# Optimization experiments

Hardware: AMD Instinct MI355X
Metric: run time of the kernel (lower is better)

The kernel has to match this reference:

```python
import jax, jax.numpy as jnp
import numpy as np

DEPTH = 10
B, F = 8192, 512
NUM_INTERNAL = 2 ** DEPTH - 1   # 1023
NUM_LEAVES = 2 ** DEPTH         # 1024
LEAF_DIMS = 64


def setup_inputs() -> dict:
    key = jax.random.key(0)
    k1, k2, k3 = jax.random.split(key, 3)
    x = jax.random.normal(k1, (B, F), dtype=jnp.float32)
    # All internal-node Dense(1) gates batched into one weight matrix [F, num_internal].
    W = jax.random.normal(k2, (F, NUM_INTERNAL), dtype=jnp.float32) * (1.0 / np.sqrt(F))
    b = jnp.zeros((NUM_INTERNAL,), dtype=jnp.float32)
    leaves_weights = jax.random.normal(k3, (NUM_LEAVES, LEAF_DIMS), dtype=jnp.float32)
    return {"x": x, "W": W, "b": b, "leaves_weights": leaves_weights}


def reference(x, W, b, leaves_weights):
    # All gate probabilities in one fused matmul + sigmoid: [B, num_internal].
    # Node i's gate is column i (BFS / level order, same as the original list of Dense layers).
    p = jax.nn.sigmoid(x @ W + b)
    batch = x.shape[0]
    # Level-by-level probability propagation. prob has shape [B, 2^lvl]:
    # the path probability of each node at the current level.
    prob = jnp.ones((batch, 1), dtype=x.dtype)
    for lvl in range(DEPTH):
        start = 2 ** lvl - 1                      # first node index at this level
        p_lvl = p[:, start:start + 2 ** lvl]      # [B, 2^lvl] gate probs at this level
        # left child gets p * prob, right child gets (1-p) * prob, interleaved in node order
        prob = jnp.stack([p_lvl * prob, (1.0 - p_lvl) * prob], axis=-1)
        prob = prob.reshape(batch, 2 ** (lvl + 1))
    # Leaf-weighted sum: sum_l prob[:, l] * leaves_weights[l, :] -> [B, leaf_dims]
    return prob @ leaves_weights
```

## Files before the change

### kernel.cpp

```cpp
#include <hip/hip_runtime.h>


typedef short bf16x8 __attribute__((ext_vector_type(8)));
typedef float f32x4 __attribute__((ext_vector_type(4)));

#define GLOAD16(g, l) __builtin_amdgcn_global_load_lds( \
    (const __attribute__((address_space(1))) void*)(g), \
    (__attribute__((address_space(3))) void*)(l), 16, 0, 0)

__device__ __forceinline__ unsigned short f2bf(float f) {
    unsigned u = __float_as_uint(f);
    return (unsigned short)((u + 0x7FFFu + ((u >> 16) & 1u)) >> 16);
}

__global__ __launch_bounds__(256) void convert_split(const float* __restrict__ x,
                                                     const float* __restrict__ W,
                                                     unsigned short* __restrict__ xh,
                                                     unsigned short* __restrict__ xl,
                                                     unsigned short* __restrict__ wh,
                                                     unsigned short* __restrict__ wl)
{
    __shared__ float tile[32][33];
    const int b = blockIdx.x;
    const int tid = threadIdx.x;
    if (b < 1024) {
        const float4* xs = reinterpret_cast<const float4*>(x);
        #pragma unroll
        for (int i = 0; i < 4; ++i) {
            const int idx = b * 1024 + i * 256 + tid;
            const float4 v = xs[idx];
            ushort4 h, l;
            h.x = f2bf(v.x); l.x = f2bf(v.x - __uint_as_float((unsigned)h.x << 16));
            h.y = f2bf(v.y); l.y = f2bf(v.y - __uint_as_float((unsigned)h.y << 16));
            h.z = f2bf(v.z); l.z = f2bf(v.z - __uint_as_float((unsigned)h.z << 16));
            h.w = f2bf(v.w); l.w = f2bf(v.w - __uint_as_float((unsigned)h.w << 16));
            reinterpret_cast<ushort4*>(xh)[idx] = h;
            reinterpret_cast<ushort4*>(xl)[idx] = l;
        }
    } else {
        const int tb = b - 1024;
        const int k0 = (tb >> 5) * 32;
        const int n0 = (tb & 31) * 32;
        const int tk = tid >> 5, tn = tid & 31;
        #pragma unroll
        for (int j = 0; j < 4; ++j) {
            const int k = k0 + tk + j * 8;
            const int n = n0 + tn;
            tile[tk + j * 8][tn] = (n < 1023) ? W[(size_t)k * 1023 + n] : 0.f;
        }
        __syncthreads();
        const int wn = tid >> 5, wk = tid & 31;
        #pragma unroll
        for (int j = 0; j < 4; ++j) {
            const int n = n0 + wn + j * 8;
            const float v = tile[wk][wn + j * 8];
            const unsigned short h = f2bf(v);
            const unsigned short lo = f2bf(v - __uint_as_float((unsigned)h << 16));
            wh[(size_t)n * 512 + k0 + wk] = h;
            wl[(size_t)n * 512 + k0 + wk] = lo;
        }
    }
}

__global__ __launch_bounds__(256, 2) void gemm_sig_mfma(
    const unsigned short* __restrict__ xh, const unsigned short* __restrict__ xl,
    const unsigned short* __restrict__ wh, const unsigned short* __restrict__ wl,
    const float* __restrict__ bias, float* __restrict__ p)
{
    __shared__ __align__(16) unsigned short Ah[128 * 32];
    __shared__ __align__(16) unsigned short Al[128 * 32];
    __shared__ __align__(16) unsigned short Bh[128 * 32];
    __shared__ __align__(16) unsigned short Bl[128 * 32];

    const int tid = threadIdx.x;
    const int lane = tid & 63;
    const int wv = tid >> 6;
    const int m_base = blockIdx.y * 128;
    const int n_base = blockIdx.x * 128;
    const int wr = wv >> 1, wc = wv & 1;

    f32x4 acc[4][4];
    #pragma unroll
    for (int i = 0; i < 4; ++i)
        #pragma unroll
        for (int j = 0; j < 4; ++j)
            acc[i][j] = (f32x4){0.f, 0.f, 0.f, 0.f};

    const int c0 = tid, c1 = tid + 256;
    const int lb0 = wv * 512;
    const int lb1 = 2048 + wv * 512;
    const int a0row = c0 >> 2, a0kc = (c0 & 3) * 8;
    const int a1row = c1 >> 2, a1kc = (c1 & 3) * 8;

    const int l15 = lane & 15, kg = lane >> 4;

    for (int k0 = 0; k0 < 512; k0 += 32) {
        GLOAD16(xh + (size_t)(m_base + a0row) * 512 + k0 + a0kc, Ah + lb0);
        GLOAD16(xh + (size_t)(m_base + a1row) * 512 + k0 + a1kc, Ah + lb1);
        GLOAD16(xl + (size_t)(m_base + a0row) * 512 + k0 + a0kc, Al + lb0);
        GLOAD16(xl + (size_t)(m_base + a1row) * 512 + k0 + a1kc, Al + lb1);
        GLOAD16(wh + (size_t)(n_base + a0row) * 512 + k0 + a0kc, Bh + lb0);
        GLOAD16(wh + (size_t)(n_base + a1row) * 512 + k0 + a1kc, Bh + lb1);
        GLOAD16(wl + (size_t)(n_base + a0row) * 512 + k0 + a0kc, Bl + lb0);
        GLOAD16(wl + (size_t)(n_base + a1row) * 512 + k0 + a1kc, Bl + lb1);
        __syncthreads();

        bf16x8 ah[4], al[4], bh[4], bl[4];
        #pragma unroll
        for (int mi = 0; mi < 4; ++mi) {
            const int off = (wr * 64 + mi * 16 + l15) * 32 + kg * 8;
            ah[mi] = *reinterpret_cast<const bf16x8*>(&Ah[off]);
            al[mi] = *reinterpret_cast<const bf16x8*>(&Al[off]);
        }
        #pragma unroll
        for (int ni = 0; ni < 4; ++ni) {
            const int off = (wc * 64 + ni * 16 + l15) * 32 + kg * 8;
            bh[ni] = *reinterpret_cast<const bf16x8*>(&Bh[off]);
            bl[ni] = *reinterpret_cast<const bf16x8*>(&Bl[off]);
        }
        #pragma unroll
        for (int mi = 0; mi < 4; ++mi)
            #pragma unroll
            for (int ni = 0; ni < 4; ++ni) {
                acc[mi][ni] = __builtin_amdgcn_mfma_f32_16x16x32_bf16(ah[mi], bh[ni], acc[mi][ni], 0, 0, 0);
                acc[mi][ni] = __builtin_amdgcn_mfma_f32_16x16x32_bf16(ah[mi], bl[ni], acc[mi][ni], 0, 0, 0);
                acc[mi][ni] = __builtin_amdgcn_mfma_f32_16x16x32_bf16(al[mi], bh[ni], acc[mi][ni], 0, 0, 0);
            }
        __syncthreads();
    }

    const int l4 = lane >> 4;
    #pragma unroll
    for (int ni = 0; ni < 4; ++ni) {
        const int n = n_base + wc * 64 + ni * 16 + l15;
        if (n < 1023) {
            const float bv = bias[n];
            #pragma unroll
            for (int mi = 0; mi < 4; ++mi) {
                #pragma unroll
                for (int r = 0; r < 4; ++r) {
                    const int m = m_base + wr * 64 + mi * 16 + l4 * 4 + r;
                    const float v = acc[mi][ni][r] + bv;
                    p[(size_t)m * 1024 + n] = 1.f / (1.f + __expf(-v));
                }
            }
        }
    }
}

__global__ __launch_bounds__(256, 4) void gemm_sig_f32(const float* __restrict__ x,
                                                       const float* __restrict__ W,
                                                       const float* __restrict__ bias,
                                                       float* __restrict__ p)
{
    __shared__ __align__(16) float As[16][128 + 4];
    __shared__ __align__(16) float Bs[16][64 + 4];
    const int tid = threadIdx.x;
    const int m_base = blockIdx.y * 128;
    const int n_base = blockIdx.x * 64;
    const int m0 = (tid >> 4) * 8, n0 = (tid & 15) * 4;
    float acc[8][4];
    #pragma unroll
    for (int i = 0; i < 8; ++i)
        #pragma unroll
        for (int j = 0; j < 4; ++j) acc[i][j] = 0.f;
    const int arow = tid >> 2, acol = (tid & 3) * 4;
    const int bk = tid >> 4, bn = (tid & 15) * 4;
    for (int k0 = 0; k0 < 512; k0 += 16) {
        #pragma unroll
        for (int i = 0; i < 2; ++i) {
            const int row = arow + i * 64;
            const float4 a = *reinterpret_cast<const float4*>(&x[(size_t)(m_base + row) * 512 + k0 + acol]);
            As[0][(acol + 0) * 132 + row] = a.x;
            As[0][(acol + 1) * 132 + row] = a.y;
            As[0][(acol + 2) * 132 + row] = a.z;
            As[0][(acol + 3) * 132 + row] = a.w;
        }
        {
            const int gk = k0 + bk;
            #pragma unroll
            for (int j = 0; j < 4; ++j) {
                const int gn = n_base + bn + j;
                Bs[bk][bn + j] = (gn < 1023) ? W[(size_t)gk * 1023 + gn] : 0.f;
            }
        }
        __syncthreads();
        #pragma unroll
        for (int kk = 0; kk < 16; ++kk) {
            const float4 b4 = *reinterpret_cast<const float4*>(&Bs[kk][n0]);
            const float4 a0 = *reinterpret_cast<const float4*>(&As[kk][m0]);
            const float4 a1 = *reinterpret_cast<const float4*>(&As[kk][m0 + 4]);
            const float a[8] = {a0.x, a0.y, a0.z, a0.w, a1.x, a1.y, a1.z, a1.w};
            const float b[4] = {b4.x, b4.y, b4.z, b4.w};
            #pragma unroll
            for (int i = 0; i < 8; ++i)
                #pragma unroll
                for (int j = 0; j < 4; ++j)
                    acc[i][j] = fmaf(a[i], b[j], acc[i][j]);
        }
        __syncthreads();
    }
    #pragma unroll
    for (int i = 0; i < 8; ++i) {
        const int gm = m_base + m0 + i;
        #pragma unroll
        for (int j = 0; j < 4; ++j) {
            const int gn = n_base + n0 + j;
            if (gn < 1023) {
                float v = acc[i][j] + bias[gn];
                p[(size_t)gm * 1024 + gn] = 1.0f / (1.0f + __expf(-v));
            }
        }
    }
}

__global__ __launch_bounds__(256, 4) void tree_leaves(const float* __restrict__ p,
                                                      const float* __restrict__ leaves,
                                                      float* __restrict__ out)
{
    __shared__ __align__(16) float prob[8][1024];

    const int tid = threadIdx.x;
    const int row_base = blockIdx.x * 8;
    const int r = tid >> 5, s = tid & 31;
    const float* pr = p + (size_t)(row_base + r) * 1024;

    float prefix = 1.f;
    #pragma unroll
    for (int lvl = 0; lvl < 5; ++lvl) {
        const int node = (1 << lvl) - 1 + (s >> (5 - lvl));
        const float v = pr[node];
        prefix *= ((s >> (4 - lvl)) & 1) ? (1.f - v) : v;
    }

    float q1[2], q2[4], q3[8], q4[16], q5[32];
    {
        const float v = pr[31 + s];
        q1[0] = prefix * v; q1[1] = prefix * (1.f - v);
    }
    {
        const float va = pr[63 + 2 * s], vb = pr[64 + 2 * s];
        q2[0] = q1[0] * va; q2[1] = q1[0] * (1.f - va);
        q2[2] = q1[1] * vb; q2[3] = q1[1] * (1.f - vb);
    }
    #pragma unroll
    for (int j = 0; j < 4; ++j) {
        const float v = pr[127 + 4 * s + j];
        q3[2 * j] = q2[j] * v; q3[2 * j + 1] = q2[j] * (1.f - v);
    }
    #pragma unroll
    for (int j = 0; j < 8; ++j) {
        const float v = pr[255 + 8 * s + j];
        q4[2 * j] = q3[j] * v; q4[2 * j + 1] = q3[j] * (1.f - v);
    }
    #pragma unroll
    for (int j = 0; j < 16; ++j) {
        const float v = pr[511 + 16 * s + j];
        q5[2 * j] = q4[j] * v; q5[2 * j + 1] = q4[j] * (1.f - v);
    }

    const int sw = (s & 7) << 2;
    #pragma unroll
    for (int u = 0; u < 32; u += 4) {
        float4 q; q.x = q5[u]; q.y = q5[u + 1]; q.z = q5[u + 2]; q.w = q5[u + 3];
        *reinterpret_cast<float4*>(&prob[r][s * 32 + (u ^ sw)]) = q;
    }
    __syncthreads();

    const int d = tid & 63, chunk = tid >> 6;
    float acc2[8];
    #pragma unroll
    for (int i = 0; i < 8; ++i) acc2[i] = 0.f;
    const float* lvp = leaves + (size_t)(chunk << 8) * 64 + d;
    for (int i = 0; i < 256; i += 4) {
        const float l0 = lvp[(i + 0) * 64];
        const float l1 = lvp[(i + 1) * 64];
        const float l2 = lvp[(i + 2) * 64];
        const float l3 = lvp[(i + 3) * 64];
        const int base = (chunk << 8) + i;
        const int sblk = base >> 5;
        const int addr = (sblk << 5) + ((base & 31) ^ ((sblk & 7) << 2));
        #pragma unroll
        for (int r2 = 0; r2 < 8; ++r2) {
            const float4 pv = *reinterpret_cast<const float4*>(&prob[r2][addr]);
            acc2[r2] = fmaf(pv.x, l0, acc2[r2]);
            acc2[r2] = fmaf(pv.y, l1, acc2[r2]);
            acc2[r2] = fmaf(pv.z, l2, acc2[r2]);
            acc2[r2] = fmaf(pv.w, l3, acc2[r2]);
        }
    }

    __syncthreads();
    float* red = &prob[0][0];
    #pragma unroll
    for (int r2 = 0; r2 < 8; ++r2)
        red[(chunk * 8 + r2) * 64 + d] = acc2[r2];
    __syncthreads();
    if (chunk == 0) {
        #pragma unroll
        for (int r2 = 0; r2 < 8; ++r2) {
            const float sum = red[r2 * 64 + d] + red[(8 + r2) * 64 + d]
                            + red[(16 + r2) * 64 + d] + red[(24 + r2) * 64 + d];
            out[(size_t)(row_base + r2) * 64 + d] = sum;
        }
    }
}

extern "C" void kernel_launch(void* const* d_in, const int* in_sizes, int n_in,
                              void* d_out, int out_size, void* d_ws, size_t ws_size,
                              hipStream_t stream) {
    const float* x      = (const float*)d_in[0];
    const float* W      = (const float*)d_in[1];
    const float* b      = (const float*)d_in[2];
    const float* leaves = (const float*)d_in[3];
    float* out = (float*)d_out;

    float* p = (float*)d_ws;
    const size_t NEED = 52428800;

    if (ws_size >= NEED) {
        unsigned short* xh = (unsigned short*)((char*)d_ws + 33554432);
        unsigned short* xl = (unsigned short*)((char*)d_ws + 41943040);
        unsigned short* wh = (unsigned short*)((char*)d_ws + 50331648);
        unsigned short* wl = (unsigned short*)((char*)d_ws + 51380224);
        convert_split<<<1536, 256, 0, stream>>>(x, W, xh, xl, wh, wl);
        gemm_sig_mfma<<<dim3(8, 64), 256, 0, stream>>>(xh, xl, wh, wl, b, p);
    } else {
        gemm_sig_f32<<<dim3(16, 64), 256, 0, stream>>>(x, W, b, p);
    }
    tree_leaves<<<1024, 256, 0, stream>>>(p, leaves, out);
}
```

Baseline: 135.2 us.

## Double-buffer GEMM LDS tiles, shift p layout for aligned loads, re-tile leaf sum

```diff
diff --git a/kernel.cpp b/kernel.cpp
--- a/kernel.cpp
+++ b/kernel.cpp
@@ -67,10 +67,10 @@
     const unsigned short* __restrict__ wh, const unsigned short* __restrict__ wl,
     const float* __restrict__ bias, float* __restrict__ p)
 {
-    __shared__ __align__(16) unsigned short Ah[128 * 32];
-    __shared__ __align__(16) unsigned short Al[128 * 32];
-    __shared__ __align__(16) unsigned short Bh[128 * 32];
-    __shared__ __align__(16) unsigned short Bl[128 * 32];
+    __shared__ __align__(16) unsigned short Ah[2][128 * 32];
+    __shared__ __align__(16) unsigned short Al[2][128 * 32];
+    __shared__ __align__(16) unsigned short Bh[2][128 * 32];
+    __shared__ __align__(16) unsigned short Bl[2][128 * 32];
 
     const int tid = threadIdx.x;
     const int lane = tid & 63;
@@ -91,32 +91,44 @@
     const int lb1 = 2048 + wv * 512;
     const int a0row = c0 >> 2, a0kc = (c0 & 3) * 8;
     const int a1row = c1 >> 2, a1kc = (c1 & 3) * 8;
-
     const int l15 = lane & 15, kg = lane >> 4;
 
-    for (int k0 = 0; k0 < 512; k0 += 32) {
-        GLOAD16(xh + (size_t)(m_base + a0row) * 512 + k0 + a0kc, Ah + lb0);
-        GLOAD16(xh + (size_t)(m_base + a1row) * 512 + k0 + a1kc, Ah + lb1);
-        GLOAD16(xl + (size_t)(m_base + a0row) * 512 + k0 + a0kc, Al + lb0);
-        GLOAD16(xl + (size_t)(m_base + a1row) * 512 + k0 + a1kc, Al + lb1);
-        GLOAD16(wh + (size_t)(n_base + a0row) * 512 + k0 + a0kc, Bh + lb0);
-        GLOAD16(wh + (size_t)(n_base + a1row) * 512 + k0 + a1kc, Bh + lb1);
-        GLOAD16(wl + (size_t)(n_base + a0row) * 512 + k0 + a0kc, Bl + lb0);
-        GLOAD16(wl + (size_t)(n_base + a1row) * 512 + k0 + a1kc, Bl + lb1);
-        __syncthreads();
+    const size_t ga0 = (size_t)(m_base + a0row) * 512 + a0kc;
+    const size_t ga1 = (size_t)(m_base + a1row) * 512 + a1kc;
+    const size_t gb0 = (size_t)(n_base + a0row) * 512 + a0kc;
+    const size_t gb1 = (size_t)(n_base + a1row) * 512 + a1kc;
+
+    #define STAGE(buf, k0) do { \
+        GLOAD16(xh + ga0 + (k0), &Ah[buf][lb0]); \
+        GLOAD16(xh + ga1 + (k0), &Ah[buf][lb1]); \
+        GLOAD16(xl + ga0 + (k0), &Al[buf][lb0]); \
+        GLOAD16(xl + ga1 + (k0), &Al[buf][lb1]); \
+        GLOAD16(wh + gb0 + (k0), &Bh[buf][lb0]); \
+        GLOAD16(wh + gb1 + (k0), &Bh[buf][lb1]); \
+        GLOAD16(wl + gb0 + (k0), &Bl[buf][lb0]); \
+        GLOAD16(wl + gb1 + (k0), &Bl[buf][lb1]); \
+    } while (0)
+
+    STAGE(0, 0);
+    __syncthreads();
+
+    #pragma unroll
+    for (int t = 0; t < 16; ++t) {
+        const int cur = t & 1;
+        if (t < 15) STAGE(cur ^ 1, (t + 1) * 32);
 
         bf16x8 ah[4], al[4], bh[4], bl[4];
         #pragma unroll
         for (int mi = 0; mi < 4; ++mi) {
             const int off = (wr * 64 + mi * 16 + l15) * 32 + kg * 8;
-            ah[mi] = *reinterpret_cast<const bf16x8*>(&Ah[off]);
-            al[mi] = *reinterpret_cast<const bf16x8*>(&Al[off]);
+            ah[mi] = *reinterpret_cast<const bf16x8*>(&Ah[cur][off]);
+            al[mi] = *reinterpret_cast<const bf16x8*>(&Al[cur][off]);
         }
         #pragma unroll
         for (int ni = 0; ni < 4; ++ni) {
             const int off = (wc * 64 + ni * 16 + l15) * 32 + kg * 8;
-            bh[ni] = *reinterpret_cast<const bf16x8*>(&Bh[off]);
-            bl[ni] = *reinterpret_cast<const bf16x8*>(&Bl[off]);
+            bh[ni] = *reinterpret_cast<const bf16x8*>(&Bh[cur][off]);
+            bl[ni] = *reinterpret_cast<const bf16x8*>(&Bl[cur][off]);
         }
         #pragma unroll
         for (int mi = 0; mi < 4; ++mi)
@@ -128,6 +140,7 @@
             }
         __syncthreads();
     }
+    #undef STAGE
 
     const int l4 = lane >> 4;
     #pragma unroll
@@ -141,7 +154,7 @@
                 for (int r = 0; r < 4; ++r) {
                     const int m = m_base + wr * 64 + mi * 16 + l4 * 4 + r;
                     const float v = acc[mi][ni][r] + bv;
-                    p[(size_t)m * 1024 + n] = 1.f / (1.f + __expf(-v));
+                    p[(size_t)m * 1024 + 1 + n] = 1.f / (1.f + __expf(-v));
                 }
             }
         }
@@ -208,7 +221,7 @@
             const int gn = n_base + n0 + j;
             if (gn < 1023) {
                 float v = acc[i][j] + bias[gn];
-                p[(size_t)gm * 1024 + gn] = 1.0f / (1.0f + __expf(-v));
+                p[(size_t)gm * 1024 + 1 + gn] = 1.0f / (1.0f + __expf(-v));
             }
         }
     }
@@ -228,35 +241,48 @@
     float prefix = 1.f;
     #pragma unroll
     for (int lvl = 0; lvl < 5; ++lvl) {
-        const int node = (1 << lvl) - 1 + (s >> (5 - lvl));
-        const float v = pr[node];
+        const float v = pr[(1 << lvl) + (s >> (5 - lvl))];
         prefix *= ((s >> (4 - lvl)) & 1) ? (1.f - v) : v;
     }
 
     float q1[2], q2[4], q3[8], q4[16], q5[32];
     {
-        const float v = pr[31 + s];
+        const float v = pr[32 + s];
         q1[0] = prefix * v; q1[1] = prefix * (1.f - v);
     }
     {
-        const float va = pr[63 + 2 * s], vb = pr[64 + 2 * s];
-        q2[0] = q1[0] * va; q2[1] = q1[0] * (1.f - va);
-        q2[2] = q1[1] * vb; q2[3] = q1[1] * (1.f - vb);
-    }
-    #pragma unroll
-    for (int j = 0; j < 4; ++j) {
-        const float v = pr[127 + 4 * s + j];
-        q3[2 * j] = q2[j] * v; q3[2 * j + 1] = q2[j] * (1.f - v);
-    }
-    #pragma unroll
-    for (int j = 0; j < 8; ++j) {
-        const float v = pr[255 + 8 * s + j];
-        q4[2 * j] = q3[j] * v; q4[2 * j + 1] = q3[j] * (1.f - v);
-    }
-    #pragma unroll
-    for (int j = 0; j < 16; ++j) {
-        const float v = pr[511 + 16 * s + j];
-        q5[2 * j] = q4[j] * v; q5[2 * j + 1] = q4[j] * (1.f - v);
+        const float2 v2 = *reinterpret_cast<const float2*>(&pr[64 + 2 * s]);
+        q2[0] = q1[0] * v2.x; q2[1] = q1[0] * (1.f - v2.x);
+        q2[2] = q1[1] * v2.y; q2[3] = q1[1] * (1.f - v2.y);
+    }
+    {
+        const float4 v4 = *reinterpret_cast<const float4*>(&pr[128 + 4 * s]);
+        const float v[4] = {v4.x, v4.y, v4.z, v4.w};
+        #pragma unroll
+        for (int j = 0; j < 4; ++j) {
+            q3[2 * j] = q2[j] * v[j]; q3[2 * j + 1] = q2[j] * (1.f - v[j]);
+        }
+    }
+    {
+        const float4 va = *reinterpret_cast<const float4*>(&pr[256 + 8 * s]);
+        const float4 vb = *reinterpret_cast<const float4*>(&pr[260 + 8 * s]);
+        const float v[8] = {va.x, va.y, va.z, va.w, vb.x, vb.y, vb.z, vb.w};
+        #pragma unroll
+        for (int j = 0; j < 8; ++j) {
+            q4[2 * j] = q3[j] * v[j]; q4[2 * j + 1] = q3[j] * (1.f - v[j]);
+        }
+    }
+    {
+        float v[16];
+        #pragma unroll
+        for (int u = 0; u < 4; ++u) {
+            const float4 vv = *reinterpret_cast<const float4*>(&pr[512 + 16 * s + 4 * u]);
+            v[4 * u] = vv.x; v[4 * u + 1] = vv.y; v[4 * u + 2] = vv.z; v[4 * u + 3] = vv.w;
+        }
+        #pragma unroll
+        for (int j = 0; j < 16; ++j) {
+            q5[2 * j] = q4[j] * v[j]; q5[2 * j + 1] = q4[j] * (1.f - v[j]);
+        }
     }
 
     const int sw = (s & 7) << 2;
@@ -267,42 +293,54 @@
     }
     __syncthreads();
 
-    const int d = tid & 63, chunk = tid >> 6;
-    float acc2[8];
-    #pragma unroll
-    for (int i = 0; i < 8; ++i) acc2[i] = 0.f;
-    const float* lvp = leaves + (size_t)(chunk << 8) * 64 + d;
-    for (int i = 0; i < 256; i += 4) {
-        const float l0 = lvp[(i + 0) * 64];
-        const float l1 = lvp[(i + 1) * 64];
-        const float l2 = lvp[(i + 2) * 64];
-        const float l3 = lvp[(i + 3) * 64];
-        const int base = (chunk << 8) + i;
-        const int sblk = base >> 5;
-        const int addr = (sblk << 5) + ((base & 31) ^ ((sblk & 7) << 2));
-        #pragma unroll
-        for (int r2 = 0; r2 < 8; ++r2) {
-            const float4 pv = *reinterpret_cast<const float4*>(&prob[r2][addr]);
-            acc2[r2] = fmaf(pv.x, l0, acc2[r2]);
-            acc2[r2] = fmaf(pv.y, l1, acc2[r2]);
-            acc2[r2] = fmaf(pv.z, l2, acc2[r2]);
-            acc2[r2] = fmaf(pv.w, l3, acc2[r2]);
-        }
-    }
+    const int cg = tid >> 4, dg = tid & 15;
+    float acc[8][4];
+    #pragma unroll
+    for (int i = 0; i < 8; ++i)
+        #pragma unroll
+        for (int j = 0; j < 4; ++j) acc[i][j] = 0.f;
+
+    const float* lv_base = leaves + (size_t)(cg * 64) * 64 + dg * 4;
+    #pragma unroll 4
+    for (int i4 = 0; i4 < 16; ++i4) {
+        const int l0 = cg * 64 + i4 * 4;
+        const int m_ = (cg * 2 + (i4 >> 3)) & 7;
+        const int col = (cg * 64 + ((i4 * 4) ^ (m_ << 2)));
+        float4 lv[4];
+        #pragma unroll
+        for (int j = 0; j < 4; ++j)
+            lv[j] = *reinterpret_cast<const float4*>(&leaves[(size_t)(l0 + j) * 64 + dg * 4]);
+        #pragma unroll
+        for (int rr = 0; rr < 8; ++rr) {
+            const float4 pv = *reinterpret_cast<const float4*>(&prob[rr][col]);
+            const float pvv[4] = {pv.x, pv.y, pv.z, pv.w};
+            #pragma unroll
+            for (int j = 0; j < 4; ++j) {
+                acc[rr][0] = fmaf(pvv[j], lv[j].x, acc[rr][0]);
+                acc[rr][1] = fmaf(pvv[j], lv[j].y, acc[rr][1]);
+                acc[rr][2] = fmaf(pvv[j], lv[j].z, acc[rr][2]);
+                acc[rr][3] = fmaf(pvv[j], lv[j].w, acc[rr][3]);
+            }
+        }
+    }
+    (void)lv_base;
 
     __syncthreads();
     float* red = &prob[0][0];
     #pragma unroll
-    for (int r2 = 0; r2 < 8; ++r2)
-        red[(chunk * 8 + r2) * 64 + d] = acc2[r2];
+    for (int rr = 0; rr < 8; ++rr) {
+        float4 q; q.x = acc[rr][0]; q.y = acc[rr][1]; q.z = acc[rr][2]; q.w = acc[rr][3];
+        *reinterpret_cast<float4*>(&red[(size_t)(cg * 8 + rr) * 64 + dg * 4]) = q;
+    }
     __syncthreads();
-    if (chunk == 0) {
-        #pragma unroll
-        for (int r2 = 0; r2 < 8; ++r2) {
-            const float sum = red[r2 * 64 + d] + red[(8 + r2) * 64 + d]
-                            + red[(16 + r2) * 64 + d] + red[(24 + r2) * 64 + d];
-            out[(size_t)(row_base + r2) * 64 + d] = sum;
-        }
+    #pragma unroll
+    for (int o = tid; o < 512; o += 256) {
+        const int rr = o >> 6, d = o & 63;
+        float sum = 0.f;
+        #pragma unroll
+        for (int c = 0; c < 16; ++c)
+            sum += red[(size_t)(c * 8 + rr) * 64 + d];
+        out[(size_t)(row_base + rr) * 64 + d] = sum;
     }
 }
 
```

Measured after the change: 129.7 us. -4.0%, faster.
